# Performance work log

Measured on AMD Instinct MI355X. Metric: run time of the kernel, lower is better.

The kernel has to match this reference:

```python
import jax, jax.numpy as jnp
import numpy as np

T, H = 8192, 2048


def setup_inputs() -> dict:
    key = jax.random.key(0)
    k1, k2, k3 = jax.random.split(key, 3)
    x_sequence = jax.random.normal(k1, (T, H), dtype=jnp.float32)
    lamda = jax.random.normal(k2, (H,), dtype=jnp.float32) * 0.2
    B = jax.random.normal(k3, (H, H), dtype=jnp.float32) / np.sqrt(H).astype(np.float32)
    return {"x_sequence": x_sequence, "lamda": lamda, "B": B}


def reference(x_sequence, lamda, B):
    # Batched input projection: u_t = B @ x_t for all t -> one GEMM. [T, H]
    u = x_sequence @ B.T
    # Linear diagonal recurrence h_t = lamda * h_{t-1} + u_t with h_0 = 0,
    # solved with a log-depth associative scan over (a, b) pairs where
    # combine((a1,b1),(a2,b2)) = (a2*a1, a2*b1 + b2).
    a = jnp.broadcast_to(lamda, u.shape)  # [T, H]

    def combine(c1, c2):
        a1, b1 = c1
        a2, b2 = c2
        return (a2 * a1, a2 * b1 + b2)

    _, h = jax.lax.associative_scan(combine, (a, u))
    return h  # [T, H] stacked hidden states
```

## Files before the change

### kernel.cpp

```cpp
#include <hip/hip_runtime.h>
#include <hip/hip_bf16.h>


#define TDIM 8192
#define HDIM 2048
#define BM 256
#define BN 256
#define BK 32
#define NT (HDIM / BK)
#define ASLOT 8192
#define BSLOT 8192
#define LCH 64
#define GCH (TDIM / LCH)

#define XBF_BYTES (TDIM * HDIM * 2)
#define BBF_BYTES (HDIM * HDIM * 2)
#define E_BYTES   (GCH * HDIM * 4)
#define WS_NEED   ((size_t)XBF_BYTES + BBF_BYTES + E_BYTES)

typedef float f32x4 __attribute__((ext_vector_type(4)));
typedef short s16x8 __attribute__((ext_vector_type(8)));

static __device__ __forceinline__ short f2bf(float f) {
  __bf16 b = (__bf16)f;
  return __builtin_bit_cast(short, b);
}

#define SB()   asm volatile("s_barrier" ::: "memory")
#define VMW(n) asm volatile("s_waitcnt vmcnt(" #n ")" ::: "memory")
#define GL(gp, lp)                                                            \
  __builtin_amdgcn_global_load_lds(                                           \
      (const __attribute__((address_space(1))) void*)(gp),                    \
      (__attribute__((address_space(3))) void*)(lp), 16, 0, 0)

__global__ void cvt_all(const float* __restrict__ X, const float* __restrict__ Bm,
                        short* __restrict__ Xb, short* __restrict__ Bbf) {
  const int XN8 = TDIM * HDIM / 8;
  const int BN8 = HDIM * HDIM / 8;
  const int stride = gridDim.x * blockDim.x;
  for (int i = blockIdx.x * blockDim.x + threadIdx.x; i < XN8 + BN8; i += stride) {
    const float* s;
    short* d;
    int k;
    if (i < XN8) { s = X; d = Xb; k = i; }
    else         { s = Bm; d = Bbf; k = i - XN8; }
    f32x4 a = *(const f32x4*)(s + (size_t)k * 8);
    f32x4 b = *(const f32x4*)(s + (size_t)k * 8 + 4);
    s16x8 v;
    v[0] = f2bf(a[0]); v[1] = f2bf(a[1]); v[2] = f2bf(a[2]); v[3] = f2bf(a[3]);
    v[4] = f2bf(b[0]); v[5] = f2bf(b[1]); v[6] = f2bf(b[2]); v[7] = f2bf(b[3]);
    *(s16x8*)(d + (size_t)k * 8) = v;
  }
}

__global__ __launch_bounds__(512, 2) void gemm8p(
    const short* __restrict__ Xb, const short* __restrict__ Bb,
    float* __restrict__ U) {
  extern __shared__ __align__(16) short smem[];
  short* As = smem;
  short* Bs = smem + 4 * ASLOT;

  const int wg  = blockIdx.x;
  const int swz = (wg & 7) * 32 + (wg >> 3);
  const int tm = swz >> 3;
  const int tn = swz & 7;
  const int row0 = tm * BM, col0 = tn * BN;

  const int tid  = threadIdx.x;
  const int lane = tid & 63;
  const int wid  = tid >> 6;
  const int wr = (wid >> 2) * 128;
  const int wc = (wid & 3) * 64;
  const int r16 = lane & 15;
  const int ks8 = (lane >> 4) * 8;

  int offA[8], offB[4];
#pragma unroll
  for (int m = 0; m < 8; ++m) {
    const int r = wr + m * 16 + r16;
    offA[m] = r * BK + (ks8 ^ ((r & 3) * 8));
  }
#pragma unroll
  for (int n = 0; n < 4; ++n) {
    const int r = wc + n * 16 + r16;
    offB[n] = r * BK + (ks8 ^ ((r & 3) * 8));
  }

  const int srow = tid >> 2;
  const int sg   = (tid & 3) ^ (srow & 3);
  const short* gA0 = Xb + (size_t)(row0 + srow) * HDIM + sg * 8;
  const short* gA1 = gA0 + (size_t)128 * HDIM;
  const short* gB0 = Bb + (size_t)(col0 + srow) * HDIM + sg * 8;
  const short* gB1 = gB0 + (size_t)128 * HDIM;

  f32x4 acc[8][4] = {};

#pragma unroll
  for (int k = 0; k < 3; ++k) {
    GL(gA0 + k * BK, &As[k * ASLOT + tid * 8]);
    GL(gA1 + k * BK, &As[k * ASLOT + 4096 + tid * 8]);
    GL(gB0 + k * BK, &Bs[k * BSLOT + tid * 8]);
    GL(gB1 + k * BK, &Bs[k * BSLOT + 4096 + tid * 8]);
  }
  VMW(8);
  SB();

#define ITER(J_, ST_, VMA_, SBF_) do {                                        \
    const int sc_ = (J_) & 3;                                                 \
    const int si_ = ((J_) + 3) & 3;                                           \
    const int ko_ = ((J_) + 3) * BK;                                          \
    s16x8 af[4], bfv[4];                                                      \
    _Pragma("unroll") for (int m = 0; m < 4; ++m)                             \
      af[m] = *(const s16x8*)&As[sc_ * ASLOT + offA[m]];                      \
    _Pragma("unroll") for (int n = 0; n < 4; ++n)                             \
      bfv[n] = *(const s16x8*)&Bs[sc_ * BSLOT + offB[n]];                     \
    if (ST_) {                                                                \
      GL(gA0 + ko_, &As[si_ * ASLOT + tid * 8]);                              \
      GL(gA1 + ko_, &As[si_ * ASLOT + 4096 + tid * 8]);                       \
    }                                                                         \
    SB();                                                                     \
    __builtin_amdgcn_s_setprio(1);                                            \
    _Pragma("unroll") for (int m = 0; m < 4; ++m)                             \
      _Pragma("unroll") for (int n = 0; n < 4; ++n)                           \
        acc[m][n] = __builtin_amdgcn_mfma_f32_16x16x32_bf16(                  \
            af[m], bfv[n], acc[m][n], 0, 0, 0);                               \
    __builtin_amdgcn_s_setprio(0);                                            \
    SB();                                                                     \
    _Pragma("unroll") for (int m = 0; m < 4; ++m)                             \
      af[m] = *(const s16x8*)&As[sc_ * ASLOT + offA[4 + m]];                  \
    if (ST_) {                                                                \
      GL(gB0 + ko_, &Bs[si_ * BSLOT + tid * 8]);                              \
      GL(gB1 + ko_, &Bs[si_ * BSLOT + 4096 + tid * 8]);                       \
    }                                                                         \
    SB();                                                                     \
    __builtin_amdgcn_s_setprio(1);                                            \
    _Pragma("unroll") for (int m = 0; m < 4; ++m)                             \
      _Pragma("unroll") for (int n = 0; n < 4; ++n)                           \
        acc[4 + m][n] = __builtin_amdgcn_mfma_f32_16x16x32_bf16(              \
            af[m], bfv[n], acc[4 + m][n], 0, 0, 0);                           \
    __builtin_amdgcn_s_setprio(0);                                            \
    VMA_;                                                                     \
    SBF_;                                                                     \
  } while (0)

#pragma unroll 4
  for (int j = 0; j < NT - 4; ++j) ITER(j, true, VMW(8), SB());
  ITER(NT - 4, true,  VMW(8), SB());
  ITER(NT - 3, false, VMW(4), SB());
  ITER(NT - 2, false, VMW(0), SB());
  ITER(NT - 1, false, (void)0, (void)0);
#undef ITER

  const int crow = row0 + wr + ((lane >> 4) << 2);
  const int ccol = col0 + wc + r16;
#pragma unroll
  for (int m = 0; m < 8; ++m)
#pragma unroll
    for (int n = 0; n < 4; ++n)
#pragma unroll
      for (int j = 0; j < 4; ++j)
        U[(size_t)(crow + m * 16 + j) * HDIM + ccol + n * 16] = acc[m][n][j];
}

__global__ __launch_bounds__(256, 2) void gemm_f32_fb(
    const float* __restrict__ X, const float* __restrict__ Bm,
    float* __restrict__ U) {
#define LDK 40
#define FBM 128
#define FBN 128
  __shared__ __align__(16) short As[2][FBM * LDK];
  __shared__ __align__(16) short Bs[2][FBN * LDK];
  const int wg  = blockIdx.x;
  const int cpx = (TDIM / FBM) * (HDIM / FBN) / 8;
  const int swz = (wg & 7) * cpx + (wg >> 3);
  const int tm = swz >> 4;
  const int tn = swz & 15;
  const int row0 = tm * FBM, col0 = tn * FBN;
  const int tid  = threadIdx.x;
  const int lane = tid & 63;
  const int wid  = tid >> 6;
  const int wr = (wid >> 1) * 64;
  const int wc = (wid & 1) * 64;
  const int srow = tid >> 2;
  const int sk   = (tid & 3) << 3;
  const float* gA  = X  + (size_t)(row0 + srow) * HDIM + sk;
  const float* gA2 = gA + 64 * HDIM;
  const float* gB  = Bm + (size_t)(col0 + srow) * HDIM + sk;
  const float* gB2 = gB + 64 * HDIM;
  f32x4 a00, a01, a10, a11, b00, b01, b10, b11;
#define LOADREG(kt) do {                                                      \
    const float* p;                                                           \
    p = gA  + (kt) * BK; a00 = *(const f32x4*)p; a01 = *(const f32x4*)(p + 4);\
    p = gA2 + (kt) * BK; a10 = *(const f32x4*)p; a11 = *(const f32x4*)(p + 4);\
    p = gB  + (kt) * BK; b00 = *(const f32x4*)p; b01 = *(const f32x4*)(p + 4);\
    p = gB2 + (kt) * BK; b10 = *(const f32x4*)p; b11 = *(const f32x4*)(p + 4);\
  } while (0)
#define CVT8(v, lo, hi) do {                                                  \
    v[0] = f2bf(lo[0]); v[1] = f2bf(lo[1]); v[2] = f2bf(lo[2]);               \
    v[3] = f2bf(lo[3]); v[4] = f2bf(hi[0]); v[5] = f2bf(hi[1]);               \
    v[6] = f2bf(hi[2]); v[7] = f2bf(hi[3]);                                   \
  } while (0)
#define DSWRITE(buf) do {                                                     \
    s16x8 v;                                                                  \
    CVT8(v, a00, a01); *(s16x8*)&As[buf][srow * LDK + sk] = v;                \
    CVT8(v, a10, a11); *(s16x8*)&As[buf][(srow + 64) * LDK + sk] = v;         \
    CVT8(v, b00, b01); *(s16x8*)&Bs[buf][srow * LDK + sk] = v;                \
    CVT8(v, b10, b11); *(s16x8*)&Bs[buf][(srow + 64) * LDK + sk] = v;         \
  } while (0)
  f32x4 acc[4][4] = {};
#define COMPUTE(buf) do {                                                     \
    const int r16_ = lane & 15;                                               \
    const int ks_  = (lane >> 4) * 8;                                         \
    s16x8 af[4], bfr[4];                                                      \
    _Pragma("unroll") for (int m = 0; m < 4; ++m)                             \
      af[m] = *(const s16x8*)&As[buf][(wr + m * 16 + r16_) * LDK + ks_];      \
    _Pragma("unroll") for (int n = 0; n < 4; ++n)                             \
      bfr[n] = *(const s16x8*)&Bs[buf][(wc + n * 16 + r16_) * LDK + ks_];     \
    _Pragma("unroll") for (int m = 0; m < 4; ++m)                             \
      _Pragma("unroll") for (int n = 0; n < 4; ++n)                           \
        acc[m][n] = __builtin_amdgcn_mfma_f32_16x16x32_bf16(                  \
            af[m], bfr[n], acc[m][n], 0, 0, 0);                               \
  } while (0)
  LOADREG(0);
  DSWRITE(0);
  __syncthreads();
#pragma unroll 2
  for (int kt = 0; kt < NT; ++kt) {
    const int cur = kt & 1;
    if (kt + 1 < NT) LOADREG(kt + 1);
    COMPUTE(cur);
    if (kt + 1 < NT) DSWRITE(cur ^ 1);
    __syncthreads();
  }
  const int crow = wr + ((lane >> 4) << 2);
  const int ccol = wc + (lane & 15);
#pragma unroll
  for (int m = 0; m < 4; ++m)
#pragma unroll
    for (int n = 0; n < 4; ++n)
#pragma unroll
      for (int j = 0; j < 4; ++j)
        U[(size_t)(row0 + crow + m * 16 + j) * HDIM + (col0 + ccol + n * 16)] =
            acc[m][n][j];
#undef LOADREG
#undef CVT8
#undef DSWRITE
#undef COMPUTE
#undef LDK
#undef FBM
#undef FBN
}

__global__ void scan_pass1(const float* __restrict__ U,
                           const float* __restrict__ lam,
                           float* __restrict__ e) {
  const int c = (blockIdx.y * 256 + threadIdx.x) * 4;
  const int j = blockIdx.x;
  const f32x4 l4 = *(const f32x4*)&lam[c];
  f32x4 h = {0.f, 0.f, 0.f, 0.f};
  const float* up = U + (size_t)j * LCH * HDIM + c;
#pragma unroll 4
  for (int t = 0; t < LCH; ++t) {
    f32x4 u4 = *(const f32x4*)up;
    h = l4 * h + u4;
    up += HDIM;
  }
  *(f32x4*)&e[(size_t)j * HDIM + c] = h;
}

__global__ void scan_carry(float* __restrict__ e, const float* __restrict__ lam) {
  const int c = (blockIdx.x * 256 + threadIdx.x) * 4;
  const f32x4 l4 = *(const f32x4*)&lam[c];
  f32x4 p = l4;
#pragma unroll
  for (int i = 0; i < 6; ++i) p = p * p;
  f32x4 E = {0.f, 0.f, 0.f, 0.f};
  for (int j = 0; j < GCH; ++j) {
    f32x4 ej = *(const f32x4*)&e[(size_t)j * HDIM + c];
    *(f32x4*)&e[(size_t)j * HDIM + c] = E;
    E = p * E + ej;
  }
}

__global__ void scan_pass3(float* __restrict__ U, const float* __restrict__ lam,
                           const float* __restrict__ carry) {
  const int c = (blockIdx.y * 256 + threadIdx.x) * 4;
  const int j = blockIdx.x;
  const f32x4 l4 = *(const f32x4*)&lam[c];
  f32x4 h = *(const f32x4*)&carry[(size_t)j * HDIM + c];
  float* up = U + (size_t)j * LCH * HDIM + c;
#pragma unroll 4
  for (int t = 0; t < LCH; ++t) {
    f32x4 u4 = *(const f32x4*)up;
    h = l4 * h + u4;
    *(f32x4*)up = h;
    up += HDIM;
  }
}

extern "C" void kernel_launch(void* const* d_in, const int* in_sizes, int n_in,
                              void* d_out, int out_size, void* d_ws, size_t ws_size,
                              hipStream_t stream) {
  const float* X   = (const float*)d_in[0];
  const float* lam = (const float*)d_in[1];
  const float* Bm  = (const float*)d_in[2];
  float* U = (float*)d_out;

  if (ws_size >= WS_NEED) {
    short* Xb = (short*)d_ws;
    short* Bb = (short*)((char*)d_ws + XBF_BYTES);
    float* e  = (float*)((char*)d_ws + XBF_BYTES + BBF_BYTES);

    hipFuncSetAttribute((const void*)gemm8p,
                        hipFuncAttributeMaxDynamicSharedMemorySize, 131072);

    cvt_all<<<dim3(4096), dim3(256), 0, stream>>>(X, Bm, Xb, Bb);
    gemm8p<<<dim3((TDIM / BM) * (HDIM / BN)), dim3(512), 131072, stream>>>(Xb, Bb, U);
    scan_pass1<<<dim3(GCH, HDIM / 1024), dim3(256), 0, stream>>>(U, lam, e);
    scan_carry<<<dim3(HDIM / 1024), dim3(256), 0, stream>>>(e, lam);
    scan_pass3<<<dim3(GCH, HDIM / 1024), dim3(256), 0, stream>>>(U, lam, e);
  } else {
    float* e = (float*)d_ws;
    gemm_f32_fb<<<dim3((TDIM / 128) * (HDIM / 128)), dim3(256), 0, stream>>>(X, Bm, U);
    scan_pass1<<<dim3(GCH, HDIM / 1024), dim3(256), 0, stream>>>(U, lam, e);
    scan_carry<<<dim3(HDIM / 1024), dim3(256), 0, stream>>>(e, lam);
    scan_pass3<<<dim3(GCH, HDIM / 1024), dim3(256), 0, stream>>>(U, lam, e);
  }
}
```

Before: 132.1 us.

## Fuse X fp32-to-bf16 conversion into GEMM A-tile loads, drop separate X convert

Removes the standalone conversion of the large X activation matrix to bf16 and instead loads fp32 X tiles into registers inside the GEMM, converting and writing them to LDS while the MFMAs run. Only B is still pre-converted through a global-load-to-LDS path. The K tile grows to 64 with a two-slot LDS ring and a new XOR swizzle, and there are fewer barriers per iteration. This saves writing and re-reading a 32MB bf16 copy of X. The cost is higher register pressure, VALU conversion work inside the main loop, and a shallower prefetch pipeline.

```diff
diff --git a/kernel.cpp b/kernel.cpp
--- a/kernel.cpp
+++ b/kernel.cpp
@@ -6,17 +6,15 @@
 #define HDIM 2048
 #define BM 256
 #define BN 256
-#define BK 32
-#define NT (HDIM / BK)
-#define ASLOT 8192
-#define BSLOT 8192
+#define KT 64
+#define NIT (HDIM / KT)
+#define SLOT 16384
 #define LCH 64
 #define GCH (TDIM / LCH)
 
-#define XBF_BYTES (TDIM * HDIM * 2)
 #define BBF_BYTES (HDIM * HDIM * 2)
 #define E_BYTES   (GCH * HDIM * 4)
-#define WS_NEED   ((size_t)XBF_BYTES + BBF_BYTES + E_BYTES)
+#define WS_NEED   ((size_t)BBF_BYTES + E_BYTES)
 
 typedef float f32x4 __attribute__((ext_vector_type(4)));
 typedef short s16x8 __attribute__((ext_vector_type(8)));
@@ -26,39 +24,31 @@
   return __builtin_bit_cast(short, b);
 }
 
-#define SB()   asm volatile("s_barrier" ::: "memory")
-#define VMW(n) asm volatile("s_waitcnt vmcnt(" #n ")" ::: "memory")
-#define GL(gp, lp)                                                            \
+#define SBAR()  asm volatile("s_barrier" ::: "memory")
+#define VMW(n)  asm volatile("s_waitcnt vmcnt(" #n ")" ::: "memory")
+#define LGKM0() asm volatile("s_waitcnt lgkmcnt(0)" ::: "memory")
+#define SCHED0() __builtin_amdgcn_sched_barrier(0)
+#define GLDS(gp, lp)                                                          \
   __builtin_amdgcn_global_load_lds(                                           \
       (const __attribute__((address_space(1))) void*)(gp),                    \
       (__attribute__((address_space(3))) void*)(lp), 16, 0, 0)
 
-__global__ void cvt_all(const float* __restrict__ X, const float* __restrict__ Bm,
-                        short* __restrict__ Xb, short* __restrict__ Bbf) {
-  const int XN8 = TDIM * HDIM / 8;
-  const int BN8 = HDIM * HDIM / 8;
-  const int stride = gridDim.x * blockDim.x;
-  for (int i = blockIdx.x * blockDim.x + threadIdx.x; i < XN8 + BN8; i += stride) {
-    const float* s;
-    short* d;
-    int k;
-    if (i < XN8) { s = X; d = Xb; k = i; }
-    else         { s = Bm; d = Bbf; k = i - XN8; }
-    f32x4 a = *(const f32x4*)(s + (size_t)k * 8);
-    f32x4 b = *(const f32x4*)(s + (size_t)k * 8 + 4);
-    s16x8 v;
-    v[0] = f2bf(a[0]); v[1] = f2bf(a[1]); v[2] = f2bf(a[2]); v[3] = f2bf(a[3]);
-    v[4] = f2bf(b[0]); v[5] = f2bf(b[1]); v[6] = f2bf(b[2]); v[7] = f2bf(b[3]);
-    *(s16x8*)(d + (size_t)k * 8) = v;
-  }
-}
-
-__global__ __launch_bounds__(512, 2) void gemm8p(
-    const short* __restrict__ Xb, const short* __restrict__ Bb,
+__global__ void cvt_B(const float* __restrict__ src, short* __restrict__ dst) {
+  const int i = blockIdx.x * 256 + threadIdx.x;
+  f32x4 a = *(const f32x4*)(src + (size_t)i * 8);
+  f32x4 b = *(const f32x4*)(src + (size_t)i * 8 + 4);
+  s16x8 v;
+  v[0] = f2bf(a[0]); v[1] = f2bf(a[1]); v[2] = f2bf(a[2]); v[3] = f2bf(a[3]);
+  v[4] = f2bf(b[0]); v[5] = f2bf(b[1]); v[6] = f2bf(b[2]); v[7] = f2bf(b[3]);
+  *(s16x8*)(dst + (size_t)i * 8) = v;
+}
+
+__global__ __launch_bounds__(512, 2) void gemm_hyb(
+    const float* __restrict__ X, const short* __restrict__ Bb,
     float* __restrict__ U) {
   extern __shared__ __align__(16) short smem[];
   short* As = smem;
-  short* Bs = smem + 4 * ASLOT;
+  short* Bs = smem + 2 * SLOT;
 
   const int wg  = blockIdx.x;
   const int swz = (wg & 7) * 32 + (wg >> 3);
@@ -71,88 +61,105 @@
   const int wid  = tid >> 6;
   const int wr = (wid >> 2) * 128;
   const int wc = (wid & 3) * 64;
-  const int r16 = lane & 15;
-  const int ks8 = (lane >> 4) * 8;
-
+
+  const int g4 = lane >> 4;
   int offA[8], offB[4];
 #pragma unroll
   for (int m = 0; m < 8; ++m) {
-    const int r = wr + m * 16 + r16;
-    offA[m] = r * BK + (ks8 ^ ((r & 3) * 8));
+    const int r = wr + m * 16 + (lane & 15);
+    offA[m] = r * 64 + ((g4 ^ (r & 3)) << 3) + (((r >> 2) & 1) << 5);
   }
 #pragma unroll
   for (int n = 0; n < 4; ++n) {
-    const int r = wc + n * 16 + r16;
-    offB[n] = r * BK + (ks8 ^ ((r & 3) * 8));
-  }
-
-  const int srow = tid >> 2;
-  const int sg   = (tid & 3) ^ (srow & 3);
-  const short* gA0 = Xb + (size_t)(row0 + srow) * HDIM + sg * 8;
-  const short* gA1 = gA0 + (size_t)128 * HDIM;
-  const short* gB0 = Bb + (size_t)(col0 + srow) * HDIM + sg * 8;
-  const short* gB1 = gB0 + (size_t)128 * HDIM;
-
-  f32x4 acc[8][4] = {};
-
-#pragma unroll
-  for (int k = 0; k < 3; ++k) {
-    GL(gA0 + k * BK, &As[k * ASLOT + tid * 8]);
-    GL(gA1 + k * BK, &As[k * ASLOT + 4096 + tid * 8]);
-    GL(gB0 + k * BK, &Bs[k * BSLOT + tid * 8]);
-    GL(gB1 + k * BK, &Bs[k * BSLOT + 4096 + tid * 8]);
-  }
-  VMW(8);
-  SB();
-
-#define ITER(J_, ST_, VMA_, SBF_) do {                                        \
-    const int sc_ = (J_) & 3;                                                 \
-    const int si_ = ((J_) + 3) & 3;                                           \
-    const int ko_ = ((J_) + 3) * BK;                                          \
-    s16x8 af[4], bfv[4];                                                      \
-    _Pragma("unroll") for (int m = 0; m < 4; ++m)                             \
-      af[m] = *(const s16x8*)&As[sc_ * ASLOT + offA[m]];                      \
+    const int r = wc + n * 16 + (lane & 15);
+    offB[n] = r * 64 + ((g4 ^ (r & 3)) << 3) + (((r >> 2) & 1) << 5);
+  }
+
+  const int trow = tid >> 3;
+  const int slog = (tid & 7) ^ (trow & 7);
+  const float* gA = X  + (size_t)(row0 + trow) * HDIM + slog * 8;
+  const short* gB = Bb + (size_t)(col0 + trow) * HDIM + slog * 8;
+
+#define ISSUE_A(dst, t_) do {                                                 \
+    _Pragma("unroll") for (int c = 0; c < 4; ++c) {                           \
+      const float* p = gA + (size_t)c * 64 * HDIM + (t_) * KT;                \
+      dst[2 * c]     = *(const f32x4*)p;                                      \
+      dst[2 * c + 1] = *(const f32x4*)(p + 4);                                \
+    }                                                                         \
+  } while (0)
+
+#define CVTWR_A(arr, sl) do {                                                 \
+    _Pragma("unroll") for (int c = 0; c < 4; ++c) {                           \
+      s16x8 v;                                                                \
+      v[0] = f2bf(arr[2*c][0]); v[1] = f2bf(arr[2*c][1]);                     \
+      v[2] = f2bf(arr[2*c][2]); v[3] = f2bf(arr[2*c][3]);                     \
+      v[4] = f2bf(arr[2*c+1][0]); v[5] = f2bf(arr[2*c+1][1]);                 \
+      v[6] = f2bf(arr[2*c+1][2]); v[7] = f2bf(arr[2*c+1][3]);                 \
+      *(s16x8*)&As[(sl) * SLOT + (c * 512 + tid) * 8] = v;                    \
+    }                                                                         \
+  } while (0)
+
+#define GLOADB(sl, t_) do {                                                   \
+    _Pragma("unroll") for (int c = 0; c < 4; ++c)                             \
+      GLDS(gB + (size_t)c * 64 * HDIM + (t_) * KT,                            \
+           &Bs[(sl) * SLOT + (c * 512 + tid) * 8]);                           \
+  } while (0)
+
+#define PHASE(sl, khx) do {                                                   \
+    s16x8 af[8], bfv[4];                                                      \
+    _Pragma("unroll") for (int m = 0; m < 8; ++m)                             \
+      af[m] = *(const s16x8*)&As[(sl) * SLOT + (offA[m] ^ (khx))];            \
     _Pragma("unroll") for (int n = 0; n < 4; ++n)                             \
-      bfv[n] = *(const s16x8*)&Bs[sc_ * BSLOT + offB[n]];                     \
-    if (ST_) {                                                                \
-      GL(gA0 + ko_, &As[si_ * ASLOT + tid * 8]);                              \
-      GL(gA1 + ko_, &As[si_ * ASLOT + 4096 + tid * 8]);                       \
-    }                                                                         \
-    SB();                                                                     \
+      bfv[n] = *(const s16x8*)&Bs[(sl) * SLOT + (offB[n] ^ (khx))];           \
     __builtin_amdgcn_s_setprio(1);                                            \
-    _Pragma("unroll") for (int m = 0; m < 4; ++m)                             \
+    _Pragma("unroll") for (int m = 0; m < 8; ++m)                             \
       _Pragma("unroll") for (int n = 0; n < 4; ++n)                           \
         acc[m][n] = __builtin_amdgcn_mfma_f32_16x16x32_bf16(                  \
             af[m], bfv[n], acc[m][n], 0, 0, 0);                               \
     __builtin_amdgcn_s_setprio(0);                                            \
-    SB();                                                                     \
-    _Pragma("unroll") for (int m = 0; m < 4; ++m)                             \
-      af[m] = *(const s16x8*)&As[sc_ * ASLOT + offA[4 + m]];                  \
-    if (ST_) {                                                                \
-      GL(gB0 + ko_, &Bs[si_ * BSLOT + tid * 8]);                              \
-      GL(gB1 + ko_, &Bs[si_ * BSLOT + 4096 + tid * 8]);                       \
-    }                                                                         \
-    SB();                                                                     \
-    __builtin_amdgcn_s_setprio(1);                                            \
-    _Pragma("unroll") for (int m = 0; m < 4; ++m)                             \
-      _Pragma("unroll") for (int n = 0; n < 4; ++n)                           \
-        acc[4 + m][n] = __builtin_amdgcn_mfma_f32_16x16x32_bf16(              \
-            af[m], bfv[n], acc[4 + m][n], 0, 0, 0);                           \
-    __builtin_amdgcn_s_setprio(0);                                            \
-    VMA_;                                                                     \
-    SBF_;                                                                     \
-  } while (0)
-
-#pragma unroll 4
-  for (int j = 0; j < NT - 4; ++j) ITER(j, true, VMW(8), SB());
-  ITER(NT - 4, true,  VMW(8), SB());
-  ITER(NT - 3, false, VMW(4), SB());
-  ITER(NT - 2, false, VMW(0), SB());
-  ITER(NT - 1, false, (void)0, (void)0);
-#undef ITER
+  } while (0)
+
+#define ITER(cur, CUR, OTH, i_) do {                                          \
+    GLOADB((cur) ^ 1, (i_) + 1);                                              \
+    SCHED0();                                                                 \
+    ISSUE_A(OTH, (i_) + 2);                                                   \
+    PHASE(cur, 0);                                                            \
+    CVTWR_A(CUR, (cur) ^ 1);                                                  \
+    PHASE(cur, 32);                                                           \
+    VMW(8);                                                                   \
+    LGKM0();                                                                  \
+    SBAR();                                                                   \
+  } while (0)
+
+  f32x4 acc[8][4] = {};
+  f32x4 SA[8], SB[8];
+
+  ISSUE_A(SA, 0);
+  GLOADB(0, 0);
+  SCHED0();
+  CVTWR_A(SA, 0);
+  ISSUE_A(SA, 1);
+  VMW(8);
+  LGKM0();
+  SBAR();
+
+#pragma unroll 1
+  for (int j = 0; j < NIT - 2; j += 2) {
+    ITER(0, SA, SB, j);
+    ITER(1, SB, SA, j + 1);
+  }
+  GLOADB(1, NIT - 1);
+  PHASE(0, 0);
+  CVTWR_A(SA, 1);
+  PHASE(0, 32);
+  VMW(0);
+  LGKM0();
+  SBAR();
+  PHASE(1, 0);
+  PHASE(1, 32);
 
   const int crow = row0 + wr + ((lane >> 4) << 2);
-  const int ccol = col0 + wc + r16;
+  const int ccol = col0 + wc + (lane & 15);
 #pragma unroll
   for (int m = 0; m < 8; ++m)
 #pragma unroll
@@ -160,6 +167,12 @@
 #pragma unroll
       for (int j = 0; j < 4; ++j)
         U[(size_t)(crow + m * 16 + j) * HDIM + ccol + n * 16] = acc[m][n][j];
+
+#undef ISSUE_A
+#undef CVTWR_A
+#undef GLOADB
+#undef PHASE
+#undef ITER
 }
 
 __global__ __launch_bounds__(256, 2) void gemm_f32_fb(
@@ -167,15 +180,16 @@
     float* __restrict__ U) {
 #define LDK 40
 #define FBM 128
-#define FBN 128
+#define FBK 32
+#define FNT (HDIM / FBK)
   __shared__ __align__(16) short As[2][FBM * LDK];
-  __shared__ __align__(16) short Bs[2][FBN * LDK];
+  __shared__ __align__(16) short Bs[2][FBM * LDK];
   const int wg  = blockIdx.x;
-  const int cpx = (TDIM / FBM) * (HDIM / FBN) / 8;
+  const int cpx = (TDIM / FBM) * (HDIM / FBM) / 8;
   const int swz = (wg & 7) * cpx + (wg >> 3);
   const int tm = swz >> 4;
   const int tn = swz & 15;
-  const int row0 = tm * FBM, col0 = tn * FBN;
+  const int row0 = tm * FBM, col0 = tn * FBM;
   const int tid  = threadIdx.x;
   const int lane = tid & 63;
   const int wid  = tid >> 6;
@@ -190,10 +204,10 @@
   f32x4 a00, a01, a10, a11, b00, b01, b10, b11;
 #define LOADREG(kt) do {                                                      \
     const float* p;                                                           \
-    p = gA  + (kt) * BK; a00 = *(const f32x4*)p; a01 = *(const f32x4*)(p + 4);\
-    p = gA2 + (kt) * BK; a10 = *(const f32x4*)p; a11 = *(const f32x4*)(p + 4);\
-    p = gB  + (kt) * BK; b00 = *(const f32x4*)p; b01 = *(const f32x4*)(p + 4);\
-    p = gB2 + (kt) * BK; b10 = *(const f32x4*)p; b11 = *(const f32x4*)(p + 4);\
+    p = gA  + (kt) * FBK; a00 = *(const f32x4*)p; a01 = *(const f32x4*)(p+4); \
+    p = gA2 + (kt) * FBK; a10 = *(const f32x4*)p; a11 = *(const f32x4*)(p+4); \
+    p = gB  + (kt) * FBK; b00 = *(const f32x4*)p; b01 = *(const f32x4*)(p+4); \
+    p = gB2 + (kt) * FBK; b10 = *(const f32x4*)p; b11 = *(const f32x4*)(p+4); \
   } while (0)
 #define CVT8(v, lo, hi) do {                                                  \
     v[0] = f2bf(lo[0]); v[1] = f2bf(lo[1]); v[2] = f2bf(lo[2]);               \
@@ -225,11 +239,11 @@
   DSWRITE(0);
   __syncthreads();
 #pragma unroll 2
-  for (int kt = 0; kt < NT; ++kt) {
+  for (int kt = 0; kt < FNT; ++kt) {
     const int cur = kt & 1;
-    if (kt + 1 < NT) LOADREG(kt + 1);
+    if (kt + 1 < FNT) LOADREG(kt + 1);
     COMPUTE(cur);
-    if (kt + 1 < NT) DSWRITE(cur ^ 1);
+    if (kt + 1 < FNT) DSWRITE(cur ^ 1);
     __syncthreads();
   }
   const int crow = wr + ((lane >> 4) << 2);
@@ -248,7 +262,8 @@
 #undef COMPUTE
 #undef LDK
 #undef FBM
-#undef FBN
+#undef FBK
+#undef FNT
 }
 
 __global__ void scan_pass1(const float* __restrict__ U,
@@ -307,21 +322,22 @@
   float* U = (float*)d_out;
 
   if (ws_size >= WS_NEED) {
-    short* Xb = (short*)d_ws;
-    short* Bb = (short*)((char*)d_ws + XBF_BYTES);
-    float* e  = (float*)((char*)d_ws + XBF_BYTES + BBF_BYTES);
-
-    hipFuncSetAttribute((const void*)gemm8p,
+    short* Bb = (short*)d_ws;
+    float* e  = (float*)((char*)d_ws + BBF_BYTES);
+
+    hipFuncSetAttribute((const void*)gemm_hyb,
                         hipFuncAttributeMaxDynamicSharedMemorySize, 131072);
 
-    cvt_all<<<dim3(4096), dim3(256), 0, stream>>>(X, Bm, Xb, Bb);
-    gemm8p<<<dim3((TDIM / BM) * (HDIM / BN)), dim3(512), 131072, stream>>>(Xb, Bb, U);
+    cvt_B<<<dim3(HDIM * HDIM / (8 * 256)), dim3(256), 0, stream>>>(Bm, Bb);
+    gemm_hyb<<<dim3((TDIM / BM) * (HDIM / BN)), dim3(512), 131072, stream>>>(
+        X, Bb, U);
     scan_pass1<<<dim3(GCH, HDIM / 1024), dim3(256), 0, stream>>>(U, lam, e);
     scan_carry<<<dim3(HDIM / 1024), dim3(256), 0, stream>>>(e, lam);
     scan_pass3<<<dim3(GCH, HDIM / 1024), dim3(256), 0, stream>>>(U, lam, e);
   } else {
     float* e = (float*)d_ws;
-    gemm_f32_fb<<<dim3((TDIM / 128) * (HDIM / 128)), dim3(256), 0, stream>>>(X, Bm, U);
+    gemm_f32_fb<<<dim3((TDIM / 128) * (HDIM / 128)), dim3(256), 0, stream>>>(
+        X, Bm, U);
     scan_pass1<<<dim3(GCH, HDIM / 1024), dim3(256), 0, stream>>>(U, lam, e);
     scan_carry<<<dim3(HDIM / 1024), dim3(256), 0, stream>>>(e, lam);
     scan_pass3<<<dim3(GCH, HDIM / 1024), dim3(256), 0, stream>>>(U, lam, e);
```

Measured after the change: 128.0 us. -3.1%, faster.
